# Optimization experiments

Measured on AMD Instinct MI355X. Metric: run time of the kernel, lower is better.

The kernel has to match this reference:

```python
import jax, jax.numpy as jnp
import numpy as np

NUM_HEADS = 12
HEAD_DIM = 64
HIDDEN = NUM_HEADS * HEAD_DIM  # 768


def setup_inputs() -> dict:
    key = jax.random.key(0)
    ks = jax.random.split(key, 18)
    B, Ni, Nt, H = 8, 1024, 512, HIDDEN
    inp = {
        "hidden_states": jax.random.normal(ks[0], (B, Ni, H), jnp.float32),
        "text": jax.random.normal(ks[1], (B, Nt, H), jnp.float32),
    }
    names = ["Wq", "Wk", "Wv", "Wqt", "Wkt", "Wvt", "Wo"]
    for i, n in enumerate(names):
        inp[n] = jax.random.normal(ks[2 + i], (H, H), jnp.float32) * 0.02
        inp["b" + n[1:]] = jnp.zeros((H,), jnp.float32)
    return inp


def _split_heads(x):
    # [B, S, H] -> [B, h, S, dh]
    B, S, _ = x.shape
    return x.reshape(B, S, NUM_HEADS, HEAD_DIM).transpose(0, 2, 1, 3)


def _merge_heads(x):
    # [B, h, S, dh] -> [B, S, H]
    B, h, S, dh = x.shape
    return x.transpose(0, 2, 1, 3).reshape(B, S, h * dh)


def _attend(q, k, v):
    scale = 1.0 / jnp.sqrt(jnp.asarray(HEAD_DIM, q.dtype))
    scores = jnp.einsum("bhqd,bhkd->bhqk", q, k) * scale
    probs = jax.nn.softmax(scores, axis=-1)
    ctx = jnp.einsum("bhqk,bhkd->bhqd", probs, v)
    return ctx, probs


def reference(hidden_states, text, Wq, bq, Wk, bk, Wv, bv,
              Wqt, bqt, Wkt, bkt, Wvt, bvt, Wo, bo):
    q_i = _split_heads(hidden_states @ Wq + bq)
    k_i = _split_heads(hidden_states @ Wk + bk)
    v_i = _split_heads(hidden_states @ Wv + bv)
    q_t = _split_heads(text @ Wqt + bqt)
    k_t = _split_heads(text @ Wkt + bkt)
    v_t = _split_heads(text @ Wvt + bvt)

    ctx_ii, weights = _attend(q_i, k_i, v_i)   # img -> img (weights returned, vis=True)
    ctx_tt, _ = _attend(q_t, k_t, v_t)         # text -> text
    ctx_it, _ = _attend(q_i, k_t, v_t)         # img queries, text keys/values
    ctx_ti, _ = _attend(q_t, k_i, v_i)         # text queries, img keys/values

    out_img = (_merge_heads(ctx_ii) + _merge_heads(ctx_it)) * 0.5 @ Wo + bo
    out_text = (_merge_heads(ctx_tt) + _merge_heads(ctx_ti)) * 0.5 @ Wo + bo
    return out_img, out_text, weights
```

## Files before the change

### kernel.cpp

```cpp
#include <hip/hip_runtime.h>

typedef __attribute__((ext_vector_type(4))) float f32x4;
typedef __attribute__((ext_vector_type(8))) short short8;
typedef __attribute__((ext_vector_type(4))) short s16x4;
typedef __attribute__((ext_vector_type(4))) unsigned short us4;
typedef unsigned short u16;
typedef unsigned char uchar;

__device__ __forceinline__ u16 f2b(float f) {
  union { float f; unsigned u; } a; a.f = f;
  unsigned r = a.u + 0x7fffu + ((a.u >> 16) & 1u);
  return (u16)(r >> 16);
}
__device__ __forceinline__ unsigned cvtpk2(float lo, float hi) {
  unsigned r;
  asm("v_cvt_pk_bf16_f32 %0, %1, %2" : "=v"(r) : "v"(lo), "v"(hi));
  return r;
}
__device__ __forceinline__ short8 cvt8(f32x4 a, f32x4 b) {
  union { unsigned u[4]; short8 s; } r;
  r.u[0] = cvtpk2(a[0], a[1]); r.u[1] = cvtpk2(a[2], a[3]);
  r.u[2] = cvtpk2(b[0], b[1]); r.u[3] = cvtpk2(b[2], b[3]);
  return r.s;
}
#define SWZ(r, byteoff) ((((r) * 128) + (byteoff)) ^ (((r) & 7) << 4))
#define C2 0.18033688011112158f

typedef __attribute__((address_space(1))) const void* gp1;
typedef __attribute__((address_space(3))) void* lp3;
__device__ __forceinline__ void gload16(const void* g, void* lds_wave_uniform_base) {
  __builtin_amdgcn_global_load_lds((gp1)g, (lp3)lds_wave_uniform_base, 16, 0, 0);
}
__device__ __forceinline__ void waitv0() { asm volatile("s_waitcnt vmcnt(0)" ::: "memory"); }
__device__ __forceinline__ void waitv1() { asm volatile("s_waitcnt vmcnt(1)" ::: "memory"); }
__device__ __forceinline__ void waitv2() { asm volatile("s_waitcnt vmcnt(2)" ::: "memory"); }
__device__ __forceinline__ void abar()  { __builtin_amdgcn_s_barrier(); }
__device__ __forceinline__ void sbar()  { __builtin_amdgcn_sched_barrier(0); }

__global__ __launch_bounds__(256) void prep_kernel(
    const float* w0, const float* w1, const float* w2, const float* w3,
    const float* w4, const float* w5, const float* w6, u16* wt,
    const float* __restrict__ h, const float* __restrict__ tx, u16* __restrict__ xb)
{
  const int bid = blockIdx.x, t = threadIdx.x;
  if (bid < 1008) {
    __shared__ float tile[64][65];
    const float* Ws[7] = {w0, w1, w2, w3, w4, w5, w6};
    int z = bid / 144, rem = bid % 144;
    const float* W = Ws[z];
    u16* out = wt + (size_t)z * 589824;
    const int r0 = (rem / 12) * 64, c0 = (rem % 12) * 64;
#pragma unroll
    for (int i = 0; i < 4; ++i) {
      int idx = i * 256 + t;
      int r = idx >> 4, c = (idx & 15) * 4;
      f32x4 v = *(const f32x4*)(W + (size_t)(r0 + r) * 768 + (c0 + c));
      tile[r][c + 0] = v[0]; tile[r][c + 1] = v[1];
      tile[r][c + 2] = v[2]; tile[r][c + 3] = v[3];
    }
    __syncthreads();
#pragma unroll
    for (int i = 0; i < 4; ++i) {
      int idx = i * 256 + t;
      int rn = idx >> 4, c = (idx & 15) * 4;
      union { us4 o; unsigned u[2]; } o;
      o.u[0] = cvtpk2(tile[c + 0][rn], tile[c + 1][rn]);
      o.u[1] = cvtpk2(tile[c + 2][rn], tile[c + 3][rn]);
      *(us4*)(out + (size_t)(c0 + rn) * 768 + (r0 + c)) = o.o;
    }
  } else {
    size_t e = ((size_t)(bid - 1008) * 256 + t) * 8;
    const float* src; size_t off;
    if (e < 6291456) { src = h; off = e; } else { src = tx; off = e - 6291456; }
    f32x4 v0 = *(const f32x4*)(src + off), v1 = *(const f32x4*)(src + off + 4);
    *(short8*)(xb + e) = cvt8(v0, v1);
  }
}

__global__ __launch_bounds__(256) void proj_kernel(
    const u16* __restrict__ Xb, const u16* __restrict__ wt,
    const float* __restrict__ bq, const float* __restrict__ bk, const float* __restrict__ bv,
    const float* __restrict__ bqt, const float* __restrict__ bkt, const float* __restrict__ bvt,
    u16* __restrict__ qi, u16* __restrict__ ki, u16* __restrict__ vti,
    u16* __restrict__ qt, u16* __restrict__ ktx, u16* __restrict__ vtt)
{
  const int bid = blockIdx.x;
  const int wk = (bid & 7) * 216 + (bid >> 3);
  const bool img = wk < 1152;
  const int id = img ? wk : wk - 1152;
  const int y = img ? (id >> 6) : (id >> 5);
  const int x = img ? (id & 63) : (id & 31);
  const int z = y / 6, n0 = (y % 6) * 128, m0 = x * 128;
  const int S = img ? 1024 : 512, logS = img ? 10 : 9;
  const u16* X = img ? Xb : Xb + 6291456;
  const u16* Wt = wt + (img ? 0 : (size_t)3 * 589824) + (size_t)y * 98304;
  const float* bias = img ? (z == 0 ? bq : z == 1 ? bk : bv)
                          : (z == 0 ? bqt : z == 1 ? bkt : bvt);
  u16* out = img ? (z == 0 ? qi : z == 1 ? ki : vti)
                 : (z == 0 ? qt : z == 1 ? ktx : vtt);
  const bool vmode = (z == 2);
  __shared__ unsigned char sm[36864];
  unsigned char* Asm = sm;
  unsigned char* Bsm = sm + 16384;
  const int t = threadIdx.x, w = t >> 6, l = t & 63;
  const int wm = (w & 1) * 64, wn = (w >> 1) * 64;
  f32x4 acc[4][4] = {};
  for (int k0 = 0; k0 < 768; k0 += 64) {
#pragma unroll
    for (int j = 0; j < 4; ++j) {
      int chunk = j * 4 + w;
      int r = chunk * 8 + (l >> 3);
      int cb = ((l & 7) * 16) ^ ((r & 7) << 4);
      gload16(X + (size_t)(m0 + r) * 768 + k0 + cb / 2, Asm + chunk * 1024);
    }
#pragma unroll
    for (int j = 0; j < 4; ++j) {
      int chunk = j * 4 + w;
      int r = chunk * 8 + (l >> 3);
      int cb = ((l & 7) * 16) ^ ((r & 7) << 4);
      gload16(Wt + (size_t)r * 768 + k0 + cb / 2, Bsm + chunk * 1024);
    }
    __syncthreads();
#pragma unroll
    for (int kc = 0; kc < 2; ++kc) {
      short8 af[4], bfr[4];
      const int koff = (kc * 32 + (l >> 4) * 8) * 2;
#pragma unroll
      for (int ms = 0; ms < 4; ++ms) {
        int row = wm + ms * 16 + (l & 15);
        af[ms] = *(const short8*)(Asm + SWZ(row, koff));
      }
#pragma unroll
      for (int ns = 0; ns < 4; ++ns) {
        int row = wn + ns * 16 + (l & 15);
        bfr[ns] = *(const short8*)(Bsm + SWZ(row, koff));
      }
      __builtin_amdgcn_s_setprio(1);
#pragma unroll
      for (int ms = 0; ms < 4; ++ms)
#pragma unroll
        for (int ns = 0; ns < 4; ++ns)
          acc[ms][ns] = __builtin_amdgcn_mfma_f32_16x16x32_bf16(af[ms], bfr[ns], acc[ms][ns], 0, 0, 0);
      __builtin_amdgcn_s_setprio(0);
    }
    __syncthreads();
  }
  float bvv[4];
#pragma unroll
  for (int ns = 0; ns < 4; ++ns) bvv[ns] = bias[n0 + wn + ns * 16 + (l & 15)];
#pragma unroll
  for (int ms = 0; ms < 4; ++ms)
#pragma unroll
    for (int ns = 0; ns < 4; ++ns)
#pragma unroll
      for (int i = 0; i < 4; ++i) {
        u16 u = f2b(acc[ms][ns][i] + bvv[ns]);
        int mm = wm + ms * 16 + (l >> 4) * 4 + i;
        int nn = wn + ns * 16 + (l & 15);
        int row = vmode ? nn : mm, col = vmode ? mm : nn;
        *(u16*)(sm + row * 272 + col * 2) = u;
      }
  __syncthreads();
  if (!vmode) {
#pragma unroll
    for (int i = 0; i < 8; ++i) {
      int idx = i * 256 + t;
      int r = idx >> 4, c = (idx & 15) * 8;
      short8 v = *(const short8*)(sm + r * 272 + c * 2);
      int sg = m0 + r, b = sg >> logS, s = sg & (S - 1);
      int n = n0 + c, hh = n >> 6, d = n & 63;
      *(short8*)(out + (((size_t)b * 12 + hh) * S + s) * 64 + d) = v;
    }
  } else {
#pragma unroll
    for (int i = 0; i < 8; ++i) {
      int idx = i * 256 + t;
      int r = idx >> 4, c = (idx & 15) * 8;
      short8 v = *(const short8*)(sm + r * 272 + c * 2);
      int n = n0 + r, hh = n >> 6, d = n & 63;
      int sg = m0 + c, b = sg >> logS, s = sg & (S - 1);
      *(short8*)(out + (((size_t)b * 12 + hh) * 64 + d) * S + s) = v;
    }
  }
}

__device__ __forceinline__ void stage_k8(const u16* Kp, int kt, uchar* Ksm, int w, int l) {
  int r = w * 8 + (l >> 3);
  int cb = ((l & 7) * 16) ^ ((r & 7) << 4);
  gload16(Kp + (size_t)(kt * 64 + r) * 64 + cb / 2, Ksm + w * 1024);
}
__device__ __forceinline__ void stage_v8(const u16* Vp, int kt, int Sk, uchar* Vsm, int w, int l) {
  int r = w * 8 + (l >> 3);
  int cb = ((l & 7) * 16) ^ ((r & 7) << 4);
  gload16(Vp + (size_t)r * Sk + kt * 64 + cb / 2, Vsm + w * 1024);
}
__device__ __forceinline__ void kfrags(const uchar* Ksm, int l, short8 kf[8]) {
#pragma unroll
  for (int kc = 0; kc < 2; ++kc)
#pragma unroll
    for (int sub = 0; sub < 4; ++sub) {
      int row = sub * 16 + (l & 15);
      kf[kc * 4 + sub] = *(const short8*)(Ksm + SWZ(row, (kc * 32 + (l >> 4) * 8) * 2));
    }
}
__device__ __forceinline__ void qk_swapped(const short8 qf[2], const short8 kf[8], f32x4 sfr[4]) {
  __builtin_amdgcn_s_setprio(1);
#pragma unroll
  for (int kc = 0; kc < 2; ++kc)
#pragma unroll
    for (int sub = 0; sub < 4; ++sub)
      sfr[sub] = __builtin_amdgcn_mfma_f32_16x16x32_bf16(kf[kc * 4 + sub], qf[kc], sfr[sub], 0, 0, 0);
  __builtin_amdgcn_s_setprio(0);
}
__device__ __forceinline__ void vfrags_sigma(const uchar* Vsm, int l, short8 vb[8]) {
#pragma unroll
  for (int kc = 0; kc < 2; ++kc)
#pragma unroll
    for (int ds = 0; ds < 4; ++ds) {
      int row = ds * 16 + (l & 15);
      union { s16x4 h[2]; short8 s; } u;
      u.h[0] = *(const s16x4*)(Vsm + SWZ(row, 64 * kc + 8 * (l >> 4)));
      u.h[1] = *(const s16x4*)(Vsm + SWZ(row, 64 * kc + 32 + 8 * (l >> 4)));
      vb[kc * 4 + ds] = u.s;
    }
}
__device__ __forceinline__ void pa_sigma(const float ps[16], short8 pa[2]) {
#pragma unroll
  for (int kc = 0; kc < 2; ++kc) {
    union { unsigned u[4]; short8 s; } r;
    r.u[0] = cvtpk2(ps[8 * kc + 0], ps[8 * kc + 1]);
    r.u[1] = cvtpk2(ps[8 * kc + 2], ps[8 * kc + 3]);
    r.u[2] = cvtpk2(ps[8 * kc + 4], ps[8 * kc + 5]);
    r.u[3] = cvtpk2(ps[8 * kc + 6], ps[8 * kc + 7]);
    pa[kc] = r.s;
  }
}
__device__ __forceinline__ void pv_sigma(const short8 pa[2], const short8 vb[8], f32x4 og[4]) {
  __builtin_amdgcn_s_setprio(1);
#pragma unroll
  for (int kc = 0; kc < 2; ++kc)
#pragma unroll
    for (int ds = 0; ds < 4; ++ds)
      og[ds] = __builtin_amdgcn_mfma_f32_16x16x32_bf16(pa[kc], vb[kc * 4 + ds], og[ds], 0, 0, 0);
  __builtin_amdgcn_s_setprio(0);
}
__device__ __forceinline__ void pass_unnorm(
    const u16* __restrict__ Kp, const u16* __restrict__ Vp, int Sk,
    const short8 qf[2], uchar* Ks0, uchar* Ks1, uchar* Vs0, uchar* Vs1,
    int w, int l, f32x4 og[4], float& ll)
{
  const int nkt = Sk >> 6;
  stage_k8(Kp, 0, Ks0, w, l);
  stage_v8(Vp, 0, Sk, Vs0, w, l);
  for (int kt = 0; kt < nkt; ++kt) {
    uchar* Kc = (kt & 1) ? Ks1 : Ks0;
    uchar* Vc = (kt & 1) ? Vs1 : Vs0;
    if (kt + 1 < nkt) {
      stage_k8(Kp, kt + 1, (kt & 1) ? Ks0 : Ks1, w, l);
      stage_v8(Vp, kt + 1, Sk, (kt & 1) ? Vs0 : Vs1, w, l);
      waitv2();
    } else {
      waitv0();
    }
    abar(); sbar();
    short8 kf[8];
    kfrags(Kc, l, kf);
    f32x4 sfr[4] = {};
    qk_swapped(qf, kf, sfr);
    float ps[16];
#pragma unroll
    for (int sub = 0; sub < 4; ++sub)
#pragma unroll
      for (int i = 0; i < 4; ++i) {
        float p = exp2f(sfr[sub][i] * C2);
        ll += p;
        ps[sub * 4 + i] = p;
      }
    short8 pa[2];
    pa_sigma(ps, pa);
    short8 vb[8];
    vfrags_sigma(Vc, l, vb);
    pv_sigma(pa, vb, og);
    sbar(); abar();
  }
}

__global__ __launch_bounds__(512, 4) void attn_kernel(
    const u16* __restrict__ qi, const u16* __restrict__ ki, const u16* __restrict__ vti,
    const u16* __restrict__ qt, const u16* __restrict__ ktx, const u16* __restrict__ vtt,
    u16* __restrict__ cimg, u16* __restrict__ ctxt, float* __restrict__ weights)
{
  __shared__ uchar smem[32768];
  const int t = threadIdx.x, w = t >> 6, l = t & 63;
  uchar* Ks0 = smem;
  uchar* Ks1 = smem + 8192;
  uchar* Vs0 = smem + 16384;
  uchar* Vs1 = smem + 24576;

  const int bid = blockIdx.x;
  const int wk = (bid & 7) * 144 + (bid >> 3);
  const bool img = wk < 768;
  const int id = img ? wk : wk - 768;
  const int x = img ? (id & 7) : (id & 3);
  const int head = img ? (id >> 3) : (id >> 2);
  const int b = head / 12, h = head % 12;
  const int Sq = img ? 1024 : 512;
  const int SkA = img ? 1024 : 512, SkB = img ? 512 : 1024;
  const u16* Qp = (img ? qi : qt) + (size_t)head * Sq * 64;
  const u16* KpA = (img ? ki : ktx) + (size_t)head * SkA * 64;
  const u16* VpA = (img ? vti : vtt) + (size_t)head * 64 * SkA;
  const u16* KpB = (img ? ktx : ki) + (size_t)head * SkB * 64;
  const u16* VpB = (img ? vtt : vti) + (size_t)head * 64 * SkB;
  u16* CTX = img ? cimg : ctxt;
  float* PROBS = img ? weights : nullptr;
  const int q0 = x * 128;
  const int qrow = q0 + w * 16 + (l & 15);

  short8 qf[2];
  qf[0] = *(const short8*)(Qp + (size_t)qrow * 64 + (l >> 4) * 8);
  qf[1] = *(const short8*)(Qp + (size_t)qrow * 64 + 32 + (l >> 4) * 8);

  f32x4 of[4] = {};
  if (PROBS) {
    float ll = 0.f;
    const int nkt = SkA >> 6;
    stage_k8(KpA, 0, Ks0, w, l);
    for (int kt = 0; kt < nkt; ++kt) {
      uchar* Kc = (kt & 1) ? Ks1 : Ks0;
      if (kt + 1 < nkt) {
        stage_k8(KpA, kt + 1, (kt & 1) ? Ks0 : Ks1, w, l);
        waitv1();
      } else {
        waitv0();
      }
      abar(); sbar();
      short8 kf[8];
      kfrags(Kc, l, kf);
      f32x4 sfr[4] = {};
      qk_swapped(qf, kf, sfr);
#pragma unroll
      for (int sub = 0; sub < 4; ++sub)
#pragma unroll
        for (int i = 0; i < 4; ++i) ll += exp2f(sfr[sub][i] * C2);
      sbar(); abar();
    }
    stage_k8(KpA, 0, Ks0, w, l);
    stage_v8(VpA, 0, SkA, Vs0, w, l);
    ll += __shfl_xor(ll, 16);
    ll += __shfl_xor(ll, 32);
    const float lb = -__log2f(ll);
    float* prow = PROBS + ((size_t)head * Sq + qrow) * SkA;
    for (int kt = 0; kt < nkt; ++kt) {
      uchar* Kc = (kt & 1) ? Ks1 : Ks0;
      uchar* Vc = (kt & 1) ? Vs1 : Vs0;
      if (kt + 1 < nkt) {
        stage_k8(KpA, kt + 1, (kt & 1) ? Ks0 : Ks1, w, l);
        stage_v8(VpA, kt + 1, SkA, (kt & 1) ? Vs0 : Vs1, w, l);
        waitv2();
      } else {
        waitv0();
      }
      abar(); sbar();
      short8 kf[8];
      kfrags(Kc, l, kf);
      f32x4 sfr[4] = {};
      qk_swapped(qf, kf, sfr);
      float ps[16];
#pragma unroll
      for (int sub = 0; sub < 4; ++sub) {
#pragma unroll
        for (int i = 0; i < 4; ++i)
          ps[sub * 4 + i] = exp2f(sfr[sub][i] * C2 + lb);
        *(f32x4*)(prow + kt * 64 + sub * 16 + (l >> 4) * 4) = *(const f32x4*)&ps[sub * 4];
      }
      short8 pa[2];
      pa_sigma(ps, pa);
      short8 vb[8];
      vfrags_sigma(Vc, l, vb);
      pv_sigma(pa, vb, of);
      sbar(); abar();
    }
#pragma unroll
    for (int ds = 0; ds < 4; ++ds) of[ds] *= 0.5f;
  } else {
    float ll = 0.f;
    pass_unnorm(KpA, VpA, SkA, qf, Ks0, Ks1, Vs0, Vs1, w, l, of, ll);
    ll += __shfl_xor(ll, 16);
    ll += __shfl_xor(ll, 32);
    float r = 0.5f / ll;
#pragma unroll
    for (int i = 0; i < 4; ++i) {
      float lv = __int_as_float(__builtin_amdgcn_ds_bpermute(
          ((l >> 4) * 4 + i) * 4, __float_as_int(r)));
#pragma unroll
      for (int ds = 0; ds < 4; ++ds) of[ds][i] *= lv;
    }
  }
  {
    f32x4 og[4] = {};
    float l2 = 0.f;
    pass_unnorm(KpB, VpB, SkB, qf, Ks0, Ks1, Vs0, Vs1, w, l, og, l2);
    l2 += __shfl_xor(l2, 16);
    l2 += __shfl_xor(l2, 32);
    float r = 0.5f / l2;
#pragma unroll
    for (int i = 0; i < 4; ++i) {
      float lv = __int_as_float(__builtin_amdgcn_ds_bpermute(
          ((l >> 4) * 4 + i) * 4, __float_as_int(r)));
#pragma unroll
      for (int ds = 0; ds < 4; ++ds) of[ds][i] += og[ds][i] * lv;
    }
  }
  __syncthreads();
  {
    uchar* Wb = smem + w * 2176;
#pragma unroll
    for (int ds = 0; ds < 4; ++ds)
#pragma unroll
      for (int i = 0; i < 4; ++i)
        *(u16*)(Wb + ((l >> 4) * 4 + i) * 136 + (16 * ds + (l & 15)) * 2) = f2b(of[ds][i]);
#pragma unroll
    for (int i = 0; i < 2; ++i) {
      int it = i * 64 + l;
      int r = it >> 3, cg = it & 7;
      short8 v = *(const short8*)(Wb + r * 136 + cg * 16);
      int s = q0 + w * 16 + r;
      *(short8*)(CTX + ((size_t)b * Sq + s) * 768 + h * 64 + cg * 8) = v;
    }
  }
}

__global__ __launch_bounds__(256) void outproj_kernel(
    const u16* __restrict__ cimg, const u16* __restrict__ ctxt,
    const u16* __restrict__ Wto, const float* __restrict__ bias,
    float* __restrict__ out_img, float* __restrict__ out_text)
{
  const int bid = blockIdx.x;
  const int wk = (bid & 7) * 72 + (bid >> 3);
  const bool img = wk < 384;
  const int id = img ? wk : wk - 384;
  const int y = img ? (id >> 6) : (id >> 5);
  const int x = img ? (id & 63) : (id & 31);
  const u16* C = img ? cimg : ctxt;
  float* OUT = img ? out_img : out_text;
  const int m0 = x * 128, n0 = y * 128;
  __shared__ unsigned char sm[32768];
  unsigned char* Asm = sm;
  unsigned char* Bsm = sm + 16384;
  const int t = threadIdx.x, w = t >> 6, l = t & 63;
  const int wm = (w & 1) * 64, wn = (w >> 1) * 64;
  f32x4 acc[4][4] = {};
  for (int k0 = 0; k0 < 768; k0 += 64) {
#pragma unroll
    for (int j = 0; j < 4; ++j) {
      int chunk = j * 4 + w;
      int r = chunk * 8 + (l >> 3);
      int cb = ((l & 7) * 16) ^ ((r & 7) << 4);
      gload16(C + (size_t)(m0 + r) * 768 + k0 + cb / 2, Asm + chunk * 1024);
    }
#pragma unroll
    for (int j = 0; j < 4; ++j) {
      int chunk = j * 4 + w;
      int r = chunk * 8 + (l >> 3);
      int cb = ((l & 7) * 16) ^ ((r & 7) << 4);
      gload16(Wto + (size_t)(n0 + r) * 768 + k0 + cb / 2, Bsm + chunk * 1024);
    }
    __syncthreads();
#pragma unroll
    for (int kc = 0; kc < 2; ++kc) {
      short8 af[4], bfr[4];
      const int koff = (kc * 32 + (l >> 4) * 8) * 2;
#pragma unroll
      for (int ms = 0; ms < 4; ++ms) {
        int row = wm + ms * 16 + (l & 15);
        af[ms] = *(const short8*)(Asm + SWZ(row, koff));
      }
#pragma unroll
      for (int ns = 0; ns < 4; ++ns) {
        int row = wn + ns * 16 + (l & 15);
        bfr[ns] = *(const short8*)(Bsm + SWZ(row, koff));
      }
      __builtin_amdgcn_s_setprio(1);
#pragma unroll
      for (int ms = 0; ms < 4; ++ms)
#pragma unroll
        for (int ns = 0; ns < 4; ++ns)
          acc[ms][ns] = __builtin_amdgcn_mfma_f32_16x16x32_bf16(af[ms], bfr[ns], acc[ms][ns], 0, 0, 0);
      __builtin_amdgcn_s_setprio(0);
    }
    __syncthreads();
  }
#pragma unroll
  for (int ms = 0; ms < 4; ++ms)
#pragma unroll
    for (int ns = 0; ns < 4; ++ns) {
      float bv = bias[n0 + wn + ns * 16 + (l & 15)];
#pragma unroll
      for (int i = 0; i < 4; ++i) {
        int mm = m0 + wm + ms * 16 + (l >> 4) * 4 + i;
        int nn = n0 + wn + ns * 16 + (l & 15);
        OUT[(size_t)mm * 768 + nn] = acc[ms][ns][i] + bv;
      }
    }
}

extern "C" void kernel_launch(void* const* d_in, const int* in_sizes, int n_in,
                              void* d_out, int out_size, void* d_ws, size_t ws_size,
                              hipStream_t stream)
{
  const float* hidden = (const float*)d_in[0];
  const float* text   = (const float*)d_in[1];
  const float* Wq  = (const float*)d_in[2];  const float* bq  = (const float*)d_in[3];
  const float* Wk  = (const float*)d_in[4];  const float* bk  = (const float*)d_in[5];
  const float* Wv  = (const float*)d_in[6];  const float* bv  = (const float*)d_in[7];
  const float* Wqt = (const float*)d_in[8];  const float* bqt = (const float*)d_in[9];
  const float* Wkt = (const float*)d_in[10]; const float* bkt = (const float*)d_in[11];
  const float* Wvt = (const float*)d_in[12]; const float* bvt = (const float*)d_in[13];
  const float* Wo  = (const float*)d_in[14]; const float* bo  = (const float*)d_in[15];

  u16* wt   = (u16*)d_ws;
  u16* xb   = wt + 7 * 589824;
  u16* qi   = xb + 9437184;
  u16* ki   = qi + 6291456;
  u16* vti  = ki + 6291456;
  u16* qt   = vti + 6291456;
  u16* ktx  = qt + 3145728;
  u16* vtt  = ktx + 3145728;
  u16* cimg = vtt + 3145728;
  u16* ctxt = cimg + 6291456;

  float* out_img  = (float*)d_out;
  float* out_text = out_img + 6291456;
  float* weights  = out_text + 3145728;

  prep_kernel<<<5616, 256, 0, stream>>>(Wq, Wk, Wv, Wqt, Wkt, Wvt, Wo, wt,
                                        hidden, text, xb);
  proj_kernel<<<1728, 256, 0, stream>>>(xb, wt, bq, bk, bv, bqt, bkt, bvt,
                                        qi, ki, vti, qt, ktx, vtt);
  attn_kernel<<<1152, 512, 0, stream>>>(qi, ki, vti, qt, ktx, vtt,
                                        cimg, ctxt, weights);
  outproj_kernel<<<576, 256, 0, stream>>>(cimg, ctxt, wt + 6 * 589824, bo,
                                          out_img, out_text);
}
```

Before: 323.4 us.

## Fuse img-text cross-attention pass into the img denominator pre-pass

For image query blocks, the text-key cross-attention pass now runs inside the first loop that computes the softmax denominator over image keys. Both K streams and the text V stream are staged together with separate double buffers. This removes a separate loop, with its barriers and pipeline fill, and overlaps the exp-only pre-pass with MFMA work. Shared memory per block grows from 32KB to 48KB, which may lower occupancy below the 4 blocks per CU requested, and register pressure rises from the extra accumulators.

```diff
diff --git a/kernel.cpp b/kernel.cpp
--- a/kernel.cpp
+++ b/kernel.cpp
@@ -34,6 +34,7 @@
 __device__ __forceinline__ void waitv0() { asm volatile("s_waitcnt vmcnt(0)" ::: "memory"); }
 __device__ __forceinline__ void waitv1() { asm volatile("s_waitcnt vmcnt(1)" ::: "memory"); }
 __device__ __forceinline__ void waitv2() { asm volatile("s_waitcnt vmcnt(2)" ::: "memory"); }
+__device__ __forceinline__ void waitv3() { asm volatile("s_waitcnt vmcnt(3)" ::: "memory"); }
 __device__ __forceinline__ void abar()  { __builtin_amdgcn_s_barrier(); }
 __device__ __forceinline__ void sbar()  { __builtin_amdgcn_sched_barrier(0); }
 
@@ -244,6 +245,27 @@
       og[ds] = __builtin_amdgcn_mfma_f32_16x16x32_bf16(pa[kc], vb[kc * 4 + ds], og[ds], 0, 0, 0);
   __builtin_amdgcn_s_setprio(0);
 }
+__device__ __forceinline__ void body_unnorm(const uchar* Kc, const uchar* Vc,
+                                            const short8 qf[2], int l, f32x4 og[4], float& ll) {
+  short8 kf[8];
+  kfrags(Kc, l, kf);
+  f32x4 sfr[4] = {};
+  qk_swapped(qf, kf, sfr);
+  float ps[16];
+#pragma unroll
+  for (int sub = 0; sub < 4; ++sub)
+#pragma unroll
+    for (int i = 0; i < 4; ++i) {
+      float p = exp2f(sfr[sub][i] * C2);
+      ll += p;
+      ps[sub * 4 + i] = p;
+    }
+  short8 pa[2];
+  pa_sigma(ps, pa);
+  short8 vb[8];
+  vfrags_sigma(Vc, l, vb);
+  pv_sigma(pa, vb, og);
+}
 __device__ __forceinline__ void pass_unnorm(
     const u16* __restrict__ Kp, const u16* __restrict__ Vp, int Sk,
     const short8 qf[2], uchar* Ks0, uchar* Ks1, uchar* Vs0, uchar* Vs1,
@@ -263,24 +285,7 @@
       waitv0();
     }
     abar(); sbar();
-    short8 kf[8];
-    kfrags(Kc, l, kf);
-    f32x4 sfr[4] = {};
-    qk_swapped(qf, kf, sfr);
-    float ps[16];
-#pragma unroll
-    for (int sub = 0; sub < 4; ++sub)
-#pragma unroll
-      for (int i = 0; i < 4; ++i) {
-        float p = exp2f(sfr[sub][i] * C2);
-        ll += p;
-        ps[sub * 4 + i] = p;
-      }
-    short8 pa[2];
-    pa_sigma(ps, pa);
-    short8 vb[8];
-    vfrags_sigma(Vc, l, vb);
-    pv_sigma(pa, vb, og);
+    body_unnorm(Kc, Vc, qf, l, og, ll);
     sbar(); abar();
   }
 }
@@ -290,7 +295,7 @@
     const u16* __restrict__ qt, const u16* __restrict__ ktx, const u16* __restrict__ vtt,
     u16* __restrict__ cimg, u16* __restrict__ ctxt, float* __restrict__ weights)
 {
-  __shared__ uchar smem[32768];
+  __shared__ uchar smem[49152];
   const int t = threadIdx.x, w = t >> 6, l = t & 63;
   uchar* Ks0 = smem;
   uchar* Ks1 = smem + 8192;
@@ -312,7 +317,6 @@
   const u16* KpB = (img ? ktx : ki) + (size_t)head * SkB * 64;
   const u16* VpB = (img ? vtt : vti) + (size_t)head * 64 * SkB;
   u16* CTX = img ? cimg : ctxt;
-  float* PROBS = img ? weights : nullptr;
   const int q0 = x * 128;
   const int qrow = q0 + w * 16 + (l & 15);
 
@@ -321,27 +325,42 @@
   qf[1] = *(const short8*)(Qp + (size_t)qrow * 64 + 32 + (l >> 4) * 8);
 
   f32x4 of[4] = {};
-  if (PROBS) {
-    float ll = 0.f;
+  if (img) {
+    uchar* Ka0 = smem;            uchar* Ka1 = smem + 8192;
+    uchar* Kb0 = smem + 16384;    uchar* Kb1 = smem + 24576;
+    uchar* Vb0 = smem + 32768;    uchar* Vb1 = smem + 40960;
+    float ll = 0.f, l2 = 0.f;
+    f32x4 og[4] = {};
     const int nkt = SkA >> 6;
-    stage_k8(KpA, 0, Ks0, w, l);
+    const int nbt = SkB >> 6;
+    stage_k8(KpA, 0, Ka0, w, l);
+    stage_k8(KpB, 0, Kb0, w, l);
+    stage_v8(VpB, 0, SkB, Vb0, w, l);
     for (int kt = 0; kt < nkt; ++kt) {
-      uchar* Kc = (kt & 1) ? Ks1 : Ks0;
-      if (kt + 1 < nkt) {
-        stage_k8(KpA, kt + 1, (kt & 1) ? Ks0 : Ks1, w, l);
-        waitv1();
-      } else {
-        waitv0();
-      }
+      uchar* Kac = (kt & 1) ? Ka1 : Ka0;
+      uchar* Kbc = (kt & 1) ? Kb1 : Kb0;
+      uchar* Vbc = (kt & 1) ? Vb1 : Vb0;
+      if (kt + 1 < nkt) stage_k8(KpA, kt + 1, (kt & 1) ? Ka0 : Ka1, w, l);
+      if (kt + 1 < nbt) {
+        stage_k8(KpB, kt + 1, (kt & 1) ? Kb0 : Kb1, w, l);
+        stage_v8(VpB, kt + 1, SkB, (kt & 1) ? Vb0 : Vb1, w, l);
+      }
+      if (kt < nbt - 1) waitv3();
+      else if (kt < nkt - 1) waitv1();
+      else waitv0();
       abar(); sbar();
-      short8 kf[8];
-      kfrags(Kc, l, kf);
-      f32x4 sfr[4] = {};
-      qk_swapped(qf, kf, sfr);
-#pragma unroll
-      for (int sub = 0; sub < 4; ++sub)
-#pragma unroll
-        for (int i = 0; i < 4; ++i) ll += exp2f(sfr[sub][i] * C2);
+      {
+        short8 kf[8];
+        kfrags(Kac, l, kf);
+        f32x4 sfr[4] = {};
+        qk_swapped(qf, kf, sfr);
+#pragma unroll
+        for (int sub = 0; sub < 4; ++sub)
+#pragma unroll
+          for (int i = 0; i < 4; ++i) ll += exp2f(sfr[sub][i] * C2);
+      }
+      if (kt < nbt)
+        body_unnorm(Kbc, Vbc, qf, l, og, l2);
       sbar(); abar();
     }
     stage_k8(KpA, 0, Ks0, w, l);
@@ -349,7 +368,10 @@
     ll += __shfl_xor(ll, 16);
     ll += __shfl_xor(ll, 32);
     const float lb = -__log2f(ll);
-    float* prow = PROBS + ((size_t)head * Sq + qrow) * SkA;
+    l2 += __shfl_xor(l2, 16);
+    l2 += __shfl_xor(l2, 32);
+    const float rB = 0.5f / l2;
+    float* prow = weights + ((size_t)head * Sq + qrow) * SkA;
     for (int kt = 0; kt < nkt; ++kt) {
       uchar* Kc = (kt & 1) ? Ks1 : Ks0;
       uchar* Vc = (kt & 1) ? Vs1 : Vs0;
@@ -382,6 +404,13 @@
     }
 #pragma unroll
     for (int ds = 0; ds < 4; ++ds) of[ds] *= 0.5f;
+#pragma unroll
+    for (int i = 0; i < 4; ++i) {
+      float lv = __int_as_float(__builtin_amdgcn_ds_bpermute(
+          ((l >> 4) * 4 + i) * 4, __float_as_int(rB)));
+#pragma unroll
+      for (int ds = 0; ds < 4; ++ds) of[ds][i] += og[ds][i] * lv;
+    }
   } else {
     float ll = 0.f;
     pass_unnorm(KpA, VpA, SkA, qf, Ks0, Ks1, Vs0, Vs1, w, l, of, ll);
@@ -395,18 +424,16 @@
 #pragma unroll
       for (int ds = 0; ds < 4; ++ds) of[ds][i] *= lv;
     }
-  }
-  {
     f32x4 og[4] = {};
     float l2 = 0.f;
     pass_unnorm(KpB, VpB, SkB, qf, Ks0, Ks1, Vs0, Vs1, w, l, og, l2);
     l2 += __shfl_xor(l2, 16);
     l2 += __shfl_xor(l2, 32);
-    float r = 0.5f / l2;
+    float r2 = 0.5f / l2;
 #pragma unroll
     for (int i = 0; i < 4; ++i) {
       float lv = __int_as_float(__builtin_amdgcn_ds_bpermute(
-          ((l >> 4) * 4 + i) * 4, __float_as_int(r)));
+          ((l >> 4) * 4 + i) * 4, __float_as_int(r2)));
 #pragma unroll
       for (int ds = 0; ds < 4; ++ds) of[ds][i] += og[ds][i] * lv;
     }
```

New measurement: 345.6 us. 6.9% more time.
